# Performance work log

Hardware: AMD Instinct MI355X
Metric: run time of the kernel (lower is better)

Reference implementation:

```python
import jax, jax.numpy as jnp
import numpy as np

N = 20000; E = 320000; IN = 512; H = 4; C = 128; HC = H * C; SD = 2; SE = 128
NEG = 0.01      # nn.LeakyReLU default slope (post-norm activations)
ATT_NEG = 0.2   # GATv2 attention LeakyReLU slope


def _gatv2(x, wl, bl, wr, br, att, bias, src, dst, concat):
    # PyG GATv2Conv (eval mode, add_self_loops already applied to src/dst)
    n = x.shape[0]
    xl = (x @ wl.T + bl).reshape(n, H, C)   # source-side projection
    xr = (x @ wr.T + br).reshape(n, H, C)   # target-side projection
    e = jax.nn.leaky_relu(xl[src] + xr[dst], ATT_NEG)        # [Etot, H, C]
    logits = jnp.einsum('ehc,hc->eh', e, att)                # [Etot, H]
    m = jax.ops.segment_max(logits, dst, num_segments=n)     # segment softmax over dst
    ez = jnp.exp(logits - m[dst])
    denom = jax.ops.segment_sum(ez, dst, num_segments=n)
    alpha = ez / denom[dst]
    out = jax.ops.segment_sum(xl[src] * alpha[:, :, None], dst, num_segments=n)  # [n, H, C]
    out = out.reshape(n, HC) if concat else out.mean(axis=1)
    return out + bias, alpha


def _bn(x, g, b):
    # BatchNorm1d, training-mode batch statistics (biased variance), eps=1e-5
    mu = x.mean(0)
    v = x.var(0)
    return g * (x - mu) * jax.lax.rsqrt(v + 1e-5) + b


def setup_inputs() -> dict:
    key = jax.random.key(0)
    ks = jax.random.split(key, 20)
    p = lambda i, shape: jax.random.normal(ks[i], shape, jnp.float32) * 0.05
    return dict(
        x=jax.random.normal(ks[0], (N, IN), jnp.float32),
        edge_index=jax.random.randint(ks[1], (2, E), 0, N),
        spatial_coords=jax.random.uniform(ks[2], (N, SD), dtype=jnp.float32),
        w1_l=p(3, (HC, IN)), b1_l=jnp.zeros((HC,)), w1_r=p(4, (HC, IN)), b1_r=jnp.zeros((HC,)),
        att1=p(5, (H, C)), bias1=jnp.zeros((HC,)), bn1_g=jnp.ones((HC,)), bn1_b=jnp.zeros((HC,)),
        w2_l=p(6, (HC, HC)), b2_l=jnp.zeros((HC,)), w2_r=p(7, (HC, HC)), b2_r=jnp.zeros((HC,)),
        att2=p(8, (H, C)), bias2=jnp.zeros((HC,)), bn2_g=jnp.ones((HC,)), bn2_b=jnp.zeros((HC,)),
        w3_l=p(9, (HC, HC)), b3_l=jnp.zeros((HC,)), w3_r=p(10, (HC, HC)), b3_r=jnp.zeros((HC,)),
        att3=p(11, (H, C)), bias3=jnp.zeros((C,)), bn3_g=jnp.ones((C,)), bn3_b=jnp.zeros((C,)),
        sp_w1=p(12, (SE, SD)), sp_b1=jnp.zeros((SE,)),
        sp_w2=p(13, (C, SE)), sp_b2=jnp.zeros((C,)),
        mha_in_w=p(14, (3 * SE, SE)), mha_in_b=jnp.zeros((3 * SE,)),
        mha_out_w=p(15, (SE, SE)), mha_out_b=jnp.zeros((SE,)),
        gate_w=p(16, (1, 2 * C)), gate_b=jnp.zeros((1,)),
    )


def reference(x, edge_index, spatial_coords,
              w1_l, b1_l, w1_r, b1_r, att1, bias1, bn1_g, bn1_b,
              w2_l, b2_l, w2_r, b2_r, att2, bias2, bn2_g, bn2_b,
              w3_l, b3_l, w3_r, b3_r, att3, bias3, bn3_g, bn3_b,
              sp_w1, sp_b1, sp_w2, sp_b2,
              mha_in_w, mha_in_b, mha_out_w, mha_out_b,
              gate_w, gate_b):
    loop = jnp.arange(N)
    src = jnp.concatenate([edge_index[0], loop])  # add self loops (PyG default)
    dst = jnp.concatenate([edge_index[1], loop])

    h1, a1 = _gatv2(x, w1_l, b1_l, w1_r, b1_r, att1, bias1, src, dst, True)
    h1 = jax.nn.leaky_relu(_bn(h1, bn1_g, bn1_b), NEG)
    h2, a2 = _gatv2(h1, w2_l, b2_l, w2_r, b2_r, att2, bias2, src, dst, True)
    h2 = jax.nn.leaky_relu(_bn(h2, bn2_g, bn2_b), NEG)
    z, a3 = _gatv2(h2, w3_l, b3_l, w3_r, b3_r, att3, bias3, src, dst, False)
    z = jax.nn.leaky_relu(_bn(z, bn3_g, bn3_b), NEG)

    # spatial embedding MLP (Linear -> LeakyReLU -> Linear -> LeakyReLU)
    emb = jax.nn.leaky_relu(spatial_coords @ sp_w1.T + sp_b1, NEG)
    emb = jax.nn.leaky_relu(emb @ sp_w2.T + sp_b2, NEG)
    # MultiheadAttention over a length-1 sequence: softmax over a single key is 1,
    # so output = W_o (W_v e + b_v) + b_o
    wv = mha_in_w[2 * SE:]
    bv = mha_in_b[2 * SE:]
    sp = (emb @ wv.T + bv) @ mha_out_w.T + mha_out_b  # [N, C]

    gate = jax.nn.softmax(jnp.concatenate([z, sp], axis=-1) @ gate_w.T + gate_b, axis=-1)  # [N,1] (all ones: size-1 softmax, faithful to source)
    z = gate * z + (1.0 - gate) * sp
    return z, a1, a2, a3, gate
```

## Files before the change

kernel.cpp:

```cpp
#include <hip/hip_runtime.h>
#include <math.h>

#define NN 20000
#define EE 320000
#define ETOT 340000
#define DEGCAP 128

typedef __attribute__((ext_vector_type(8))) short short8;
typedef __attribute__((ext_vector_type(4))) float f32x4;

__device__ __forceinline__ float lrelu(float x, float s) { return fmaxf(x, s * x); }
__device__ __forceinline__ float bf2f(ushort u) {
    union { uint i; float f; } c;
    c.i = ((uint)u) << 16;
    return c.f;
}
__device__ __forceinline__ ushort f2bf(float f) {
    uint u = __float_as_uint(f);
    uint r = (u + 0x7FFFu + ((u >> 16) & 1u)) >> 16;
    return (ushort)r;
}
__device__ __forceinline__ void gload16(const ushort* g, ushort* l) {
    __builtin_amdgcn_global_load_lds((const __attribute__((address_space(1))) void*)g,
                                     (__attribute__((address_space(3))) void*)l, 16, 0, 0);
}

__global__ __launch_bounds__(1024) void k_scan(const int* __restrict__ counts, int* __restrict__ rstart) {
    __shared__ int sm[1024];
    int t = threadIdx.x;
    const int CH = 20;
    int base = t * CH;
    int loc[CH];
    int s = 0;
#pragma unroll
    for (int j = 0; j < CH; ++j) {
        int idx = base + j;
        int v = (idx < NN) ? counts[idx] : 0;
        loc[j] = s;
        s += v;
    }
    sm[t] = s;
    __syncthreads();
    for (int o = 1; o < 1024; o <<= 1) {
        int v = (t >= o) ? sm[t - o] : 0;
        __syncthreads();
        if (t >= o) sm[t] += v;
        __syncthreads();
    }
    int off = sm[t] - s;
#pragma unroll
    for (int j = 0; j < CH; ++j) {
        int idx = base + j;
        if (idx < NN) rstart[idx] = off + loc[j];
    }
    if (t == 1023) rstart[NN] = sm[1023];
}

__global__ void k_scatter(const int* __restrict__ ei, const int* __restrict__ rstart,
                          int* __restrict__ cursor, int* __restrict__ csr) {
    int i = blockIdx.x * blockDim.x + threadIdx.x;
    if (i >= ETOT) return;
    int d = (i < EE) ? ei[EE + i] : (i - EE);
    int pos = atomicAdd(&cursor[d], 1);
    csr[rstart[d] + pos] = i;
}

__global__ void k_prep(const float* __restrict__ x, const float* __restrict__ w0, const float* __restrict__ w1,
                       const float* __restrict__ w2, const float* __restrict__ w3, const float* __restrict__ w4,
                       const float* __restrict__ w5, ushort* __restrict__ xout, ushort* __restrict__ wout,
                       const int* __restrict__ ei, int* __restrict__ counts) {
    int b = blockIdx.x, t = threadIdx.x;
    if (b < 10000) {
        int i = (b * 256 + t) * 4;
        float4 v = *(const float4*)(x + i);
        uint2 pk;
        pk.x = (uint)f2bf(v.x) | ((uint)f2bf(v.y) << 16);
        pk.y = (uint)f2bf(v.z) | ((uint)f2bf(v.w) << 16);
        *(uint2*)(xout + i) = pk;
    } else if (b < 11536) {
        int q = (b - 10000) * 256 + t;
        if (q >= 6 * 65536) return;
        int which = q >> 16;
        int off = (q & 65535) << 2;
        const float* src = which == 0 ? w0 : which == 1 ? w1 : which == 2 ? w2 : which == 3 ? w3 : which == 4 ? w4 : w5;
        float4 v = *(const float4*)(src + off);
        uint2 pk;
        pk.x = (uint)f2bf(v.x) | ((uint)f2bf(v.y) << 16);
        pk.y = (uint)f2bf(v.z) | ((uint)f2bf(v.w) << 16);
        *(uint2*)(wout + which * 262144 + off) = pk;
    } else {
        int i = (b - 11536) * 256 + t;
        if (i >= ETOT) return;
        int d = (i < EE) ? ei[EE + i] : (i - EE);
        atomicAdd(&counts[d], 1);
    }
}

__global__ __launch_bounds__(256) void k_gemm2(const ushort* __restrict__ A, const ushort* __restrict__ W,
                                               const float* __restrict__ bl, const float* __restrict__ br,
                                               ushort* __restrict__ XL, ushort* __restrict__ XR) {
    __shared__ ushort As[2][512][8];
    __shared__ ushort Bs[2][512][8];
    int tid = threadIdx.x;
    int wid = tid >> 6, lane = tid & 63;
    int wm = wid >> 1, wn = wid & 1;
    int bid = blockIdx.x;
    int L = (bid & 7) * 157 + (bid >> 3);
    int mt = L >> 3, nt = L & 7;
    int bm = mt * 128, bn = nt * 128;
    const float* bias = (nt >= 4) ? br : bl;
    ushort* C = (nt >= 4) ? XR : XL;
    int cb = bn - ((nt >= 4) ? 512 : 0);
    int lrow = lane & 15, lslot = lane >> 4;
    int f0 = tid, f1 = tid + 256;
    int r0 = f0 & 127, ks0 = f0 >> 7;
    int r1 = f1 & 127, ks1 = f1 >> 7;
    int ar0 = bm + r0; if (ar0 >= NN) ar0 = NN - 1;
    int ar1 = bm + r1; if (ar1 >= NN) ar1 = NN - 1;
    const ushort* ga0 = A + (size_t)ar0 * 512 + ks0 * 8;
    const ushort* ga1 = A + (size_t)ar1 * 512 + ks1 * 8;
    const ushort* gb0 = W + (size_t)(bn + r0) * 512 + ks0 * 8;
    const ushort* gb1 = W + (size_t)(bn + r1) * 512 + ks1 * 8;
    f32x4 acc[4][4] = {};
    gload16(ga0, &As[0][f0][0]);
    gload16(ga1, &As[0][f1][0]);
    gload16(gb0, &Bs[0][f0][0]);
    gload16(gb1, &Bs[0][f1][0]);
#pragma unroll 4
    for (int t = 0; t < 16; ++t) {
        int cur = t & 1;
        __syncthreads();
        if (t < 15) {
            int k0 = (t + 1) * 32;
            int nxt = cur ^ 1;
            gload16(ga0 + k0, &As[nxt][f0][0]);
            gload16(ga1 + k0, &As[nxt][f1][0]);
            gload16(gb0 + k0, &Bs[nxt][f0][0]);
            gload16(gb1 + k0, &Bs[nxt][f1][0]);
        }
        short8 af[4], bfr[4];
#pragma unroll
        for (int i = 0; i < 4; ++i) af[i] = *(const short8*)&As[cur][lslot * 128 + wm * 64 + i * 16 + lrow][0];
#pragma unroll
        for (int j = 0; j < 4; ++j) bfr[j] = *(const short8*)&Bs[cur][lslot * 128 + wn * 64 + j * 16 + lrow][0];
#pragma unroll
        for (int i = 0; i < 4; ++i)
#pragma unroll
            for (int j = 0; j < 4; ++j)
                acc[i][j] = __builtin_amdgcn_mfma_f32_16x16x32_bf16(af[i], bfr[j], acc[i][j], 0, 0, 0);
    }
#pragma unroll
    for (int i = 0; i < 4; ++i) {
#pragma unroll
        for (int j = 0; j < 4; ++j) {
            int gcol = cb + wn * 64 + j * 16 + lrow;
            float bv = bias[gcol];
            int growb = bm + wm * 64 + i * 16 + lslot * 4;
#pragma unroll
            for (int reg = 0; reg < 4; ++reg) {
                int grow = growb + reg;
                if (grow < NN) C[(size_t)grow * 512 + gcol] = f2bf(acc[i][j][reg] + bv);
            }
        }
    }
}

__global__ __launch_bounds__(256) void k_fused(const ushort* __restrict__ xl, const ushort* __restrict__ xr,
                                               const float* __restrict__ att, const int* __restrict__ ei,
                                               const int* __restrict__ rstart, const int* __restrict__ csr,
                                               const float* __restrict__ bias, float* __restrict__ alpha,
                                               ushort* __restrict__ dest, int meanHeads) {
    __shared__ float slg[4][DEGCAP][4];
    __shared__ int ssrc[4][DEGCAP];
    int w = threadIdx.x >> 6, lane = threadIdx.x & 63;
    int node = blockIdx.x * 4 + w;
    int s0 = rstart[node];
    int deg = rstart[node + 1] - s0;
    int hh = lane >> 4;
    short8 xrv = *(const short8*)(xr + (size_t)node * 512 + lane * 8);
    const float4* at = (const float4*)att + lane * 2;
    float4 a0 = at[0], a1 = at[1];
    float attv[8] = {a0.x, a0.y, a0.z, a0.w, a1.x, a1.y, a1.z, a1.w};
    float xrf[8];
#pragma unroll
    for (int j = 0; j < 8; ++j) xrf[j] = bf2f((ushort)xrv[j]);
    for (int i = lane; i < deg; i += 64) {
        int e = csr[s0 + i];
        ssrc[w][i < DEGCAP ? i : 0] = (e < EE) ? ei[e] : e - EE;
    }
    float m = -1e30f, denom = 0.f;
    float acc[8] = {};
    int scur = ssrc[w][0];
    short8 row = *(const short8*)(xl + (size_t)scur * 512 + lane * 8);
    for (int i = 0; i < deg; ++i) {
        short8 rown = row;
        if (i + 1 < deg) {
            int sn = ssrc[w][(i + 1) < DEGCAP ? (i + 1) : 0];
            rown = *(const short8*)(xl + (size_t)sn * 512 + lane * 8);
        }
        float rf[8];
#pragma unroll
        for (int j = 0; j < 8; ++j) rf[j] = bf2f((ushort)row[j]);
        float p = 0.f;
#pragma unroll
        for (int j = 0; j < 8; ++j) {
            float e = rf[j] + xrf[j];
            p = fmaf(fmaxf(e, 0.2f * e), attv[j], p);
        }
        p += __shfl_xor(p, 1);
        p += __shfl_xor(p, 2);
        p += __shfl_xor(p, 4);
        p += __shfl_xor(p, 8);
        if ((lane & 15) == 0 && i < DEGCAP) slg[w][i][hh] = p;
        if (p <= m) {
            float wg = __expf(p - m);
            denom += wg;
#pragma unroll
            for (int j = 0; j < 8; ++j) acc[j] = fmaf(wg, rf[j], acc[j]);
        } else {
            float sc = __expf(m - p);
            denom = fmaf(denom, sc, 1.f);
#pragma unroll
            for (int j = 0; j < 8; ++j) acc[j] = fmaf(acc[j], sc, rf[j]);
            m = p;
        }
        row = rown;
    }
    float rd = 1.f / denom;
    float m0 = __shfl(m, 0), m1 = __shfl(m, 16), m2 = __shfl(m, 32), m3 = __shfl(m, 48);
    float r0 = __shfl(rd, 0), r1 = __shfl(rd, 16), r2 = __shfl(rd, 32), r3 = __shfl(rd, 48);
    int nal = deg < DEGCAP ? deg : DEGCAP;
    for (int i = lane; i < nal; i += 64) {
        int e = csr[s0 + i];
        float4 l = *(const float4*)&slg[w][i][0];
        float4 av;
        av.x = __expf(l.x - m0) * r0;
        av.y = __expf(l.y - m1) * r1;
        av.z = __expf(l.z - m2) * r2;
        av.w = __expf(l.w - m3) * r3;
        *(float4*)(alpha + (size_t)e * 4) = av;
    }
#pragma unroll
    for (int j = 0; j < 8; ++j) acc[j] *= rd;
    if (!meanHeads) {
        int c = lane * 8;
        short8 o;
#pragma unroll
        for (int j = 0; j < 8; ++j) o[j] = (short)f2bf(acc[j] + bias[c + j]);
        *(short8*)(dest + (size_t)node * 512 + c) = o;
    } else {
#pragma unroll
        for (int j = 0; j < 8; ++j) {
            acc[j] += __shfl_xor(acc[j], 16);
            acc[j] += __shfl_xor(acc[j], 32);
        }
        if (lane < 16) {
            int c = lane * 8;
            short8 o;
#pragma unroll
            for (int j = 0; j < 8; ++j) o[j] = (short)f2bf(0.25f * acc[j] + bias[c + j]);
            *(short8*)(dest + (size_t)node * 128 + c) = o;
        }
    }
}

__global__ void k_bnstats(const ushort* __restrict__ X, float* __restrict__ s, float* __restrict__ s2, int npairs) {
    int t = threadIdx.x;
    if (t >= npairs) return;
    float a0 = 0.f, a1 = 0.f, q0 = 0.f, q1 = 0.f;
    for (int r = blockIdx.x; r < NN; r += gridDim.x) {
        uint p = ((const uint*)X)[r * npairs + t];
        float v0 = bf2f((ushort)(p & 0xffffu));
        float v1 = bf2f((ushort)(p >> 16));
        a0 += v0; q0 += v0 * v0;
        a1 += v1; q1 += v1 * v1;
    }
    atomicAdd(&s[2 * t], a0);
    atomicAdd(&s[2 * t + 1], a1);
    atomicAdd(&s2[2 * t], q0);
    atomicAdd(&s2[2 * t + 1], q1);
}

__global__ void k_bnapply(const ushort* __restrict__ X, const float* __restrict__ g, const float* __restrict__ b,
                          const float* __restrict__ bsum, const float* __restrict__ bsq, float* __restrict__ Yf,
                          ushort* __restrict__ Yb, float* __restrict__ gout, int mask4, int n4) {
    int i = blockIdx.x * blockDim.x + threadIdx.x;
    if (gout && i < NN) gout[i] = 1.0f;
    if (i >= n4) return;
    int c = (i & mask4) << 2;
    uint2 p = ((const uint2*)X)[i];
    float x0 = bf2f((ushort)(p.x & 0xffffu)), x1 = bf2f((ushort)(p.x >> 16));
    float x2 = bf2f((ushort)(p.y & 0xffffu)), x3 = bf2f((ushort)(p.y >> 16));
    float4 S = *(const float4*)(bsum + c);
    float4 Q = *(const float4*)(bsq + c);
    float4 G = *(const float4*)(g + c);
    float4 B = *(const float4*)(b + c);
    const float inv = 1.f / NN;
    float mx = S.x * inv, my = S.y * inv, mz = S.z * inv, mw = S.w * inv;
    float rx = rsqrtf(Q.x * inv - mx * mx + 1e-5f);
    float ry = rsqrtf(Q.y * inv - my * my + 1e-5f);
    float rz = rsqrtf(Q.z * inv - mz * mz + 1e-5f);
    float rw = rsqrtf(Q.w * inv - mw * mw + 1e-5f);
    float4 y;
    y.x = lrelu(G.x * (x0 - mx) * rx + B.x, 0.01f);
    y.y = lrelu(G.y * (x1 - my) * ry + B.y, 0.01f);
    y.z = lrelu(G.z * (x2 - mz) * rz + B.z, 0.01f);
    y.w = lrelu(G.w * (x3 - mw) * rw + B.w, 0.01f);
    if (Yb) {
        uint2 pk;
        pk.x = (uint)f2bf(y.x) | ((uint)f2bf(y.y) << 16);
        pk.y = (uint)f2bf(y.z) | ((uint)f2bf(y.w) << 16);
        *(uint2*)(Yb + (size_t)i * 4) = pk;
    } else {
        ((float4*)Yf)[i] = y;
    }
}

extern "C" void kernel_launch(void* const* d_in, const int* in_sizes, int n_in,
                              void* d_out, int out_size, void* d_ws, size_t ws_size,
                              hipStream_t stream) {
    const float* x = (const float*)d_in[0];
    const int* ei = (const int*)d_in[1];
    const float* wl[3] = {(const float*)d_in[3], (const float*)d_in[11], (const float*)d_in[19]};
    const float* bl[3] = {(const float*)d_in[4], (const float*)d_in[12], (const float*)d_in[20]};
    const float* wr[3] = {(const float*)d_in[5], (const float*)d_in[13], (const float*)d_in[21]};
    const float* br[3] = {(const float*)d_in[6], (const float*)d_in[14], (const float*)d_in[22]};
    const float* att[3] = {(const float*)d_in[7], (const float*)d_in[15], (const float*)d_in[23]};
    const float* bias[3] = {(const float*)d_in[8], (const float*)d_in[16], (const float*)d_in[24]};
    const float* bng[3] = {(const float*)d_in[9], (const float*)d_in[17], (const float*)d_in[25]};
    const float* bnb[3] = {(const float*)d_in[10], (const float*)d_in[18], (const float*)d_in[26]};

    ushort* a_bf = (ushort*)d_ws;
    ushort* xl_bf = a_bf + (size_t)NN * 512;
    ushort* xr_bf = xl_bf + (size_t)NN * 512;
    ushort* h_bf = xr_bf + (size_t)NN * 512;
    ushort* wbuf = h_bf + (size_t)NN * 512;
    float* fp = (float*)(wbuf + 6 * 262144);
    float* bsum = fp;
    float* bsq = bsum + 512;
    int* counts = (int*)(bsq + 512);
    int* cursor = counts + NN;
    int* rstart = cursor + NN;
    int* csr = rstart + (NN + 1);
    size_t need = (size_t)((char*)(csr + ETOT) - (char*)d_ws);
    if (ws_size < need) return;

    float* out = (float*)d_out;
    float* zout = out;
    float* aout[3] = {out + 2560000, out + 3920000, out + 5280000};
    float* gout = out + 6640000;

    hipMemsetAsync(counts, 0, 2 * NN * sizeof(int), stream);
    k_prep<<<12865, 256, 0, stream>>>(x, wl[0], wr[0], wl[1], wr[1], wl[2], wr[2], a_bf, wbuf, ei, counts);
    k_scan<<<1, 1024, 0, stream>>>(counts, rstart);
    k_scatter<<<(ETOT + 255) / 256, 256, 0, stream>>>(ei, rstart, cursor, csr);

    for (int l = 0; l < 3; ++l) {
        const ushort* wb = wbuf + (size_t)l * 524288;
        k_gemm2<<<1256, 256, 0, stream>>>(a_bf, wb, bl[l], br[l], xl_bf, xr_bf);
        int ncols = (l == 2) ? 128 : 512;
        k_fused<<<NN / 4, 256, 0, stream>>>(xl_bf, xr_bf, att[l], ei, rstart, csr, bias[l], aout[l], h_bf,
                                            (l == 2) ? 1 : 0);
        hipMemsetAsync(bsum, 0, 1024 * sizeof(float), stream);
        k_bnstats<<<240, 256, 0, stream>>>(h_bf, bsum, bsq, ncols / 2);
        int n4 = NN * ncols / 4;
        if (l < 2) {
            k_bnapply<<<(n4 + 255) / 256, 256, 0, stream>>>(h_bf, bng[l], bnb[l], bsum, bsq, nullptr, a_bf,
                                                            nullptr, ncols / 4 - 1, n4);
        } else {
            k_bnapply<<<(n4 + 255) / 256, 256, 0, stream>>>(h_bf, bng[l], bnb[l], bsum, bsq, zout, nullptr,
                                                            gout, ncols / 4 - 1, n4);
        }
    }
}
```

Before: 702.9 us.

## Use BK=64 single-buffered GEMM tiles and fold BN-stat zeroing into fused kernel

The GEMM now loads a 64-wide K slab per iteration into a single LDS buffer with per-wave contiguous global_load_lds chunks, then syncs around compute, instead of double-buffering 32-wide slabs. This halves the number of loop iterations and barriers per tile but gives up the overlap of the next load with the current MFMA work. Separately, block 0 of the fused attention kernel zeroes the BN accumulator buffer, which removes a hipMemsetAsync launch per layer.

Result: no change. 696.3 us (-0.9%).

```diff
diff --git a/kernel.cpp b/kernel.cpp
--- a/kernel.cpp
+++ b/kernel.cpp
@@ -20,7 +20,7 @@
     uint r = (u + 0x7FFFu + ((u >> 16) & 1u)) >> 16;
     return (ushort)r;
 }
-__device__ __forceinline__ void gload16(const ushort* g, ushort* l) {
+__device__ __forceinline__ void gload16(const ushort* g, const ushort* l) {
     __builtin_amdgcn_global_load_lds((const __attribute__((address_space(1))) void*)g,
                                      (__attribute__((address_space(3))) void*)l, 16, 0, 0);
 }
@@ -99,8 +99,8 @@
 __global__ __launch_bounds__(256) void k_gemm2(const ushort* __restrict__ A, const ushort* __restrict__ W,
                                                const float* __restrict__ bl, const float* __restrict__ br,
                                                ushort* __restrict__ XL, ushort* __restrict__ XR) {
-    __shared__ ushort As[2][512][8];
-    __shared__ ushort Bs[2][512][8];
+    __shared__ ushort As[8][128][8];
+    __shared__ ushort Bs[8][128][8];
     int tid = threadIdx.x;
     int wid = tid >> 6, lane = tid & 63;
     int wm = wid >> 1, wn = wid & 1;
@@ -112,42 +112,46 @@
     ushort* C = (nt >= 4) ? XR : XL;
     int cb = bn - ((nt >= 4) ? 512 : 0);
     int lrow = lane & 15, lslot = lane >> 4;
-    int f0 = tid, f1 = tid + 256;
-    int r0 = f0 & 127, ks0 = f0 >> 7;
-    int r1 = f1 & 127, ks1 = f1 >> 7;
-    int ar0 = bm + r0; if (ar0 >= NN) ar0 = NN - 1;
-    int ar1 = bm + r1; if (ar1 >= NN) ar1 = NN - 1;
-    const ushort* ga0 = A + (size_t)ar0 * 512 + ks0 * 8;
-    const ushort* ga1 = A + (size_t)ar1 * 512 + ks1 * 8;
-    const ushort* gb0 = W + (size_t)(bn + r0) * 512 + ks0 * 8;
-    const ushort* gb1 = W + (size_t)(bn + r1) * 512 + ks1 * 8;
+    const ushort* gA[4];
+    const ushort* gB[4];
+    const ushort* lA[4];
+    const ushort* lB[4];
+    const ushort* flatA = &As[0][0][0];
+    const ushort* flatB = &Bs[0][0][0];
+#pragma unroll
+    for (int q = 0; q < 4; ++q) {
+        int cbch = wid * 64 + 256 * q;
+        lA[q] = flatA + (size_t)cbch * 8;
+        lB[q] = flatB + (size_t)cbch * 8;
+        int c = cbch + lane;
+        int r = c & 127, ks = c >> 7;
+        int ar = bm + r;
+        if (ar >= NN) ar = NN - 1;
+        gA[q] = A + (size_t)ar * 512 + ks * 8;
+        gB[q] = W + (size_t)(bn + r) * 512 + ks * 8;
+    }
     f32x4 acc[4][4] = {};
-    gload16(ga0, &As[0][f0][0]);
-    gload16(ga1, &As[0][f1][0]);
-    gload16(gb0, &Bs[0][f0][0]);
-    gload16(gb1, &Bs[0][f1][0]);
-#pragma unroll 4
-    for (int t = 0; t < 16; ++t) {
-        int cur = t & 1;
+    for (int k0 = 0; k0 < 512; k0 += 64) {
+#pragma unroll
+        for (int q = 0; q < 4; ++q) {
+            gload16(gA[q] + k0, lA[q]);
+            gload16(gB[q] + k0, lB[q]);
+        }
         __syncthreads();
-        if (t < 15) {
-            int k0 = (t + 1) * 32;
-            int nxt = cur ^ 1;
-            gload16(ga0 + k0, &As[nxt][f0][0]);
-            gload16(ga1 + k0, &As[nxt][f1][0]);
-            gload16(gb0 + k0, &Bs[nxt][f0][0]);
-            gload16(gb1 + k0, &Bs[nxt][f1][0]);
-        }
-        short8 af[4], bfr[4];
-#pragma unroll
-        for (int i = 0; i < 4; ++i) af[i] = *(const short8*)&As[cur][lslot * 128 + wm * 64 + i * 16 + lrow][0];
-#pragma unroll
-        for (int j = 0; j < 4; ++j) bfr[j] = *(const short8*)&Bs[cur][lslot * 128 + wn * 64 + j * 16 + lrow][0];
-#pragma unroll
-        for (int i = 0; i < 4; ++i)
-#pragma unroll
-            for (int j = 0; j < 4; ++j)
-                acc[i][j] = __builtin_amdgcn_mfma_f32_16x16x32_bf16(af[i], bfr[j], acc[i][j], 0, 0, 0);
+#pragma unroll
+        for (int ks = 0; ks < 2; ++ks) {
+            short8 af[4], bfr[4];
+#pragma unroll
+            for (int i = 0; i < 4; ++i) af[i] = *(const short8*)&As[ks * 4 + lslot][wm * 64 + i * 16 + lrow][0];
+#pragma unroll
+            for (int j = 0; j < 4; ++j) bfr[j] = *(const short8*)&Bs[ks * 4 + lslot][wn * 64 + j * 16 + lrow][0];
+#pragma unroll
+            for (int i = 0; i < 4; ++i)
+#pragma unroll
+                for (int j = 0; j < 4; ++j)
+                    acc[i][j] = __builtin_amdgcn_mfma_f32_16x16x32_bf16(af[i], bfr[j], acc[i][j], 0, 0, 0);
+        }
+        __syncthreads();
     }
 #pragma unroll
     for (int i = 0; i < 4; ++i) {
@@ -169,9 +173,13 @@
                                                const float* __restrict__ att, const int* __restrict__ ei,
                                                const int* __restrict__ rstart, const int* __restrict__ csr,
                                                const float* __restrict__ bias, float* __restrict__ alpha,
-                                               ushort* __restrict__ dest, int meanHeads) {
+                                               ushort* __restrict__ dest, float* __restrict__ bzero, int meanHeads) {
     __shared__ float slg[4][DEGCAP][4];
     __shared__ int ssrc[4][DEGCAP];
+    if (blockIdx.x == 0) {
+        float4 z = {0.f, 0.f, 0.f, 0.f};
+        ((float4*)bzero)[threadIdx.x] = z;
+    }
     int w = threadIdx.x >> 6, lane = threadIdx.x & 63;
     int node = blockIdx.x * 4 + w;
     int s0 = rstart[node];
@@ -360,8 +368,7 @@
         k_gemm2<<<1256, 256, 0, stream>>>(a_bf, wb, bl[l], br[l], xl_bf, xr_bf);
         int ncols = (l == 2) ? 128 : 512;
         k_fused<<<NN / 4, 256, 0, stream>>>(xl_bf, xr_bf, att[l], ei, rstart, csr, bias[l], aout[l], h_bf,
-                                            (l == 2) ? 1 : 0);
-        hipMemsetAsync(bsum, 0, 1024 * sizeof(float), stream);
+                                            bsum, (l == 2) ? 1 : 0);
         k_bnstats<<<240, 256, 0, stream>>>(h_bf, bsum, bsq, ncols / 2);
         int n4 = NN * ncols / 4;
         if (l < 2) {
```
